# Performance work log

Measured on AMD Instinct MI355X. Metric: run time of the kernel, lower is better.

## Reference

```python
import jax, jax.numpy as jnp
import numpy as np

N_NODES = 100000


def gcn_conv(x, edge_index, W, num_nodes):
    """PyG GCNConv (bias=False): add self-loops, symmetric normalization,
    out[c] = sum_{(r,c) in E'} deg^{-1/2}[r] * deg^{-1/2}[c] * (x @ W)[r]."""
    h = x @ W  # [N, out_dim]
    row, col = edge_index[0], edge_index[1]
    loop = jnp.arange(num_nodes, dtype=row.dtype)
    row = jnp.concatenate([row, loop])
    col = jnp.concatenate([col, loop])
    ones = jnp.ones(row.shape[0], dtype=h.dtype)
    deg = jax.ops.segment_sum(ones, col, num_segments=num_nodes)  # [N]
    dinv = jnp.where(deg > 0, jax.lax.rsqrt(deg), 0.0)
    norm = dinv[row] * dinv[col]  # [E+N]
    msgs = norm[:, None] * h[row]  # gather + scale
    return jax.ops.segment_sum(msgs, col, num_segments=num_nodes)  # scatter-add


def setup_inputs() -> dict:
    key = jax.random.key(0)
    k1, k2, k3, k4 = jax.random.split(key, 4)
    x = jax.random.normal(k1, (N_NODES, 128), dtype=jnp.float32)
    edge_index = jax.random.randint(k2, (2, 3200000), 0, N_NODES, dtype=jnp.int64)
    W1 = jax.random.normal(k3, (128, 32), dtype=jnp.float32) * (1.0 / np.sqrt(128))
    W2 = jax.random.normal(k4, (32, 3), dtype=jnp.float32) * (1.0 / np.sqrt(32))
    return {"x": x, "edge_index": edge_index, "W1": W1, "W2": W2}


def reference(x, edge_index, W1, W2):
    n = x.shape[0]
    hidden1 = jnp.tanh(gcn_conv(x, edge_index, W1, n))  # dropout p=0.0 -> identity
    z = gcn_conv(hidden1, edge_index, W2, n)
    return z  # original returns (z, z, None)
```

## Files before the change

kernel.cpp:

```cpp
#include <hip/hip_runtime.h>
#include <hip/hip_fp16.h>

#define N_NODES 100000
#define N_EDGES 3200000
#define F_IN    128
#define F_HID   32

#define BSHIFT  7
#define BKSZ    128
#define NBKT    ((N_NODES + BKSZ - 1) / BKSZ)
#define CAP     4608
#define CHUNK   4096
#define NBLK_E  ((N_EDGES + CHUNK - 1) / CHUNK)
#define RBITS   17
#define RMASK   0x1FFFF


__global__ __launch_bounds__(512) void k_part(const int* __restrict__ row, const int* __restrict__ col,
                                              int* __restrict__ gcur, unsigned* __restrict__ bkt) {
    __shared__ int hist[NBKT];
    __shared__ int lbase[NBKT];
    __shared__ int gbase[NBKT];
    __shared__ unsigned perm[CHUNK];
    __shared__ unsigned short pb[CHUNK];
    __shared__ int wt[8];
    int t = threadIdx.x;
    for (int i = t; i < NBKT; i += 512) hist[i] = 0;
    __syncthreads();

    int e0 = blockIdx.x * CHUNK;
    int n  = min(CHUNK, N_EDGES - e0);
    int r[8], c[8], rk[8];
#pragma unroll
    for (int k = 0; k < 8; k++) {
        int idx = t + k * 512;
        if (idx < n) {
            r[k]  = row[e0 + idx];
            c[k]  = col[e0 + idx];
            rk[k] = atomicAdd(&hist[c[k] >> BSHIFT], 1);
        }
    }
    __syncthreads();

    {
        int b0 = t * 2;
        int s0 = (b0     < NBKT) ? hist[b0]     : 0;
        int s1 = (b0 + 1 < NBKT) ? hist[b0 + 1] : 0;
        int tsum = s0 + s1;
        int lane = t & 63, wid = t >> 6;
        int incl = tsum;
#pragma unroll
        for (int sh = 1; sh < 64; sh <<= 1) {
            int u = __shfl_up(incl, sh);
            if (lane >= sh) incl += u;
        }
        if (lane == 63) wt[wid] = incl;
        __syncthreads();
        int wpre = 0;
        for (int w = 0; w < wid; w++) wpre += wt[w];
        int excl = wpre + incl - tsum;
        if (b0     < NBKT) lbase[b0]     = excl;
        if (b0 + 1 < NBKT) lbase[b0 + 1] = excl + s0;
    }
    for (int i = t; i < NBKT; i += 512) {
        int h = hist[i];
        gbase[i] = i * CAP + (h ? atomicAdd(&gcur[i], h) : 0);
    }
    __syncthreads();

#pragma unroll
    for (int k = 0; k < 8; k++) {
        int idx = t + k * 512;
        if (idx < n) {
            int b   = c[k] >> BSHIFT;
            int pos = lbase[b] + rk[k];
            perm[pos] = (unsigned)r[k] | ((unsigned)(c[k] & (BKSZ - 1)) << RBITS);
            pb[pos]   = (unsigned short)b;
        }
    }
    __syncthreads();

    for (int i = t; i < n; i += 512) {
        int b = pb[i];
        bkt[gbase[b] + (i - lbase[b])] = perm[i];
    }
}


__global__ __launch_bounds__(1024) void k_bucket(unsigned* __restrict__ bkt,
                                                 const int* __restrict__ gcur,
                                                 int* __restrict__ off, int* __restrict__ end,
                                                 float* __restrict__ dinv) {
    __shared__ unsigned stg[CAP];
    __shared__ int cnt[BKSZ];
    __shared__ int cur[BKSZ];
    __shared__ int wtot[2];
    int t = threadIdx.x, b = blockIdx.x;
    int s = b * CAP, m = gcur[b];
    if (t < BKSZ) cnt[t] = 0;
    __syncthreads();
    for (int i = t; i < m; i += 1024) {
        unsigned x = bkt[s + i];
        stg[i] = x;
        atomicAdd(&cnt[x >> RBITS], 1);
    }
    __syncthreads();

    int lane = t & 63, wid = t >> 6;
    int v = 0, incl = 0;
    if (t < BKSZ) {
        v = cnt[t];
        incl = v;
        #pragma unroll
        for (int sh = 1; sh < 64; sh <<= 1) {
            int u = __shfl_up(incl, sh);
            if (lane >= sh) incl += u;
        }
        if (lane == 63) wtot[wid] = incl;
    }
    __syncthreads();
    if (t < BKSZ) {
        int wpre = (wid == 1) ? wtot[0] : 0;
        int excl = wpre + incl - v;
        cur[t] = s + excl;
        int g = b * BKSZ + t;
        if (g < N_NODES) {
            off[g]  = s + excl;
            end[g]  = s + excl + v;
            dinv[g] = rsqrtf((float)(v + 1));
        }
    }
    __syncthreads();
    for (int i = t; i < m; i += 1024) {
        unsigned x = stg[i];
        int p = atomicAdd(&cur[x >> RBITS], 1);
        bkt[p] = x & RMASK;
    }
}


__global__ __launch_bounds__(256) void k_gemm1(const float* __restrict__ x, const float* __restrict__ W1,
                                               const float* __restrict__ dinv, unsigned* __restrict__ h1s) {
    __shared__ float Wlds[F_IN * F_HID];
    int t = threadIdx.x;
    for (int i = t; i < F_IN * F_HID; i += 256) Wlds[i] = W1[i];
    __syncthreads();

    int gid = blockIdx.x * 256 + t;
    int r = gid >> 3, f4 = gid & 7;
    if (r >= N_NODES) return;

    const float4* x4  = (const float4*)(x + (size_t)r * F_IN);
    const float4* Wl4 = (const float4*)Wlds;
    float ax = 0.f, ay = 0.f, az = 0.f, aw = 0.f;
#pragma unroll
    for (int k4 = 0; k4 < F_IN / 4; k4++) {
        float4 xv = x4[k4];
        float4 w0 = Wl4[(4 * k4 + 0) * 8 + f4];
        ax += xv.x * w0.x; ay += xv.x * w0.y; az += xv.x * w0.z; aw += xv.x * w0.w;
        float4 w1 = Wl4[(4 * k4 + 1) * 8 + f4];
        ax += xv.y * w1.x; ay += xv.y * w1.y; az += xv.y * w1.z; aw += xv.y * w1.w;
        float4 w2 = Wl4[(4 * k4 + 2) * 8 + f4];
        ax += xv.z * w2.x; ay += xv.z * w2.y; az += xv.z * w2.z; aw += xv.z * w2.w;
        float4 w3 = Wl4[(4 * k4 + 3) * 8 + f4];
        ax += xv.w * w3.x; ay += xv.w * w3.y; az += xv.w * w3.z; aw += xv.w * w3.w;
    }
    float di = dinv[r];
    unsigned p01 = (unsigned)__half_as_ushort(__float2half(di * ax))
                 | ((unsigned)__half_as_ushort(__float2half(di * ay)) << 16);
    unsigned p23 = (unsigned)__half_as_ushort(__float2half(di * az))
                 | ((unsigned)__half_as_ushort(__float2half(di * aw)) << 16);
    ((uint2*)h1s)[(size_t)r * 8 + f4] = make_uint2(p01, p23);
}


__global__ __launch_bounds__(256) void k_conv1(const int* __restrict__ off, const int* __restrict__ end,
                                               const int* __restrict__ srt, const float* __restrict__ dinv,
                                               const unsigned* __restrict__ h1s,
                                               const float* __restrict__ W2, float* __restrict__ h2s4) {
    int wid  = threadIdx.x >> 6;
    int lane = threadIdx.x & 63;
    int c = blockIdx.x * 4 + wid;
    if (c >= N_NODES) return;
    int o = lane & 7;
    int q = lane >> 3;
    int pp = q & 1;
    int fA = 4 * o + 2 * pp, fB = fA + 1;

    float wA0 = W2[fA * 3 + 0], wA1 = W2[fA * 3 + 1], wA2 = W2[fA * 3 + 2];
    float wB0 = W2[fB * 3 + 0], wB1 = W2[fB * 3 + 1], wB2 = W2[fB * 3 + 2];

    int b = off[c], e = end[c];
    __half2 s01a = __float2half2_rn(0.0f), s23a = s01a;
    __half2 s01b = s01a, s23b = s01a;
    const uint2* h1v = (const uint2*)h1s;
    int p = b + q;
    for (; p + 8 < e; p += 16) {
        int r0 = srt[p];
        int r1 = srt[p + 8];
        uint2 v0 = h1v[(size_t)r0 * 8 + o];
        uint2 v1 = h1v[(size_t)r1 * 8 + o];
        s01a = __hadd2(s01a, *(const __half2*)&v0.x);
        s23a = __hadd2(s23a, *(const __half2*)&v0.y);
        s01b = __hadd2(s01b, *(const __half2*)&v1.x);
        s23b = __hadd2(s23b, *(const __half2*)&v1.y);
    }
    if (p < e) {
        int r0 = srt[p];
        uint2 v0 = h1v[(size_t)r0 * 8 + o];
        s01a = __hadd2(s01a, *(const __half2*)&v0.x);
        s23a = __hadd2(s23a, *(const __half2*)&v0.y);
    }
    __half2 s01 = __hadd2(s01a, s01b);
    __half2 s23 = __hadd2(s23a, s23b);

    float f0 = __low2float(s01), f1 = __high2float(s01);
    float f2v = __low2float(s23), f3 = __high2float(s23);
#pragma unroll
    for (int m = 8; m <= 32; m <<= 1) {
        f0  += __shfl_xor(f0, m);  f1 += __shfl_xor(f1, m);
        f2v += __shfl_xor(f2v, m); f3 += __shfl_xor(f3, m);
    }

    uint2 sv = h1v[(size_t)c * 8 + o];
    f0  += __low2float(*(const __half2*)&sv.x);
    f1  += __high2float(*(const __half2*)&sv.x);
    f2v += __low2float(*(const __half2*)&sv.y);
    f3  += __high2float(*(const __half2*)&sv.y);

    float di = dinv[c];
    float vA = pp ? f2v : f0;
    float vB = pp ? f3  : f1;
    float hA = tanhf(di * vA);
    float hB = tanhf(di * vB);

    float p0 = hA * wA0 + hB * wB0;
    float p1 = hA * wA1 + hB * wB1;
    float p2 = hA * wA2 + hB * wB2;
#pragma unroll
    for (int m = 1; m <= 32; m <<= 1) {
        p0 += __shfl_xor(p0, m);
        p1 += __shfl_xor(p1, m);
        p2 += __shfl_xor(p2, m);
    }
    if (lane < 4) {
        float vv = (lane == 0) ? p0 : (lane == 1) ? p1 : (lane == 2) ? p2 : 0.0f;
        h2s4[(size_t)c * 4 + lane] = (lane < 3) ? (di * 0.25f) * vv : 0.0f;
    }
}


__global__ __launch_bounds__(256) void k_conv2(const int* __restrict__ off, const int* __restrict__ end,
                                               const int* __restrict__ srt, const float* __restrict__ dinv,
                                               const float* __restrict__ h2s4, float* __restrict__ out) {
    int wid  = threadIdx.x >> 6;
    int lane = threadIdx.x & 63;
    int c = blockIdx.x * 4 + wid;
    if (c >= N_NODES) return;

    const float4* h2v = (const float4*)h2s4;
    int b = off[c], e = end[c];
    float ax = 0.0f, ay = 0.0f, az = 0.0f;
    for (int p = b + lane; p < e; p += 64) {
        int r = srt[p];
        float4 v = h2v[r];
        ax += v.x; ay += v.y; az += v.z;
    }
#pragma unroll
    for (int m = 1; m <= 32; m <<= 1) {
        ax += __shfl_xor(ax, m);
        ay += __shfl_xor(ay, m);
        az += __shfl_xor(az, m);
    }

    float di = dinv[c];
    if (lane < 3) {
        float a = (lane == 0) ? ax : (lane == 1) ? ay : az;
        out[(size_t)c * 3 + lane] = di * (a + h2s4[(size_t)c * 4 + lane]);
    }
}


extern "C" void kernel_launch(void* const* d_in, const int* in_sizes, int n_in,
                              void* d_out, int out_size, void* d_ws, size_t ws_size,
                              hipStream_t stream) {
    const float* x   = (const float*)d_in[0];
    const int*   ei  = (const int*)d_in[1];
    const float* W1  = (const float*)d_in[2];
    const float* W2  = (const float*)d_in[3];
    float*       out = (float*)d_out;

    const int* row = ei;
    const int* col = ei + N_EDGES;

    char* ws = (char*)d_ws;
    unsigned* bkt = (unsigned*)ws;
    int*      srt = (int*)ws;
    char*     p   = ws + 4ull * NBKT * CAP;
    int*      gcur = (int*)p;                 p += 4ull * ((NBKT + 63) & ~63);
    int*      off  = (int*)p;                 p += 4ull * N_NODES;
    int*      end  = (int*)p;                 p += 4ull * N_NODES;
    float*    dinv = (float*)p;               p += 4ull * N_NODES;
    unsigned* h1s  = (unsigned*)p;            p += 64ull * N_NODES;
    float*    h2s4 = (float*)p;

    const int B = 256;
    hipMemsetAsync(gcur, 0, 4ull * NBKT, stream);
    hipLaunchKernelGGL(k_part,   dim3(NBLK_E), dim3(512),  0, stream, row, col, gcur, bkt);
    hipLaunchKernelGGL(k_bucket, dim3(NBKT),   dim3(1024), 0, stream, bkt, gcur, off, end, dinv);
    hipLaunchKernelGGL(k_gemm1,  dim3((N_NODES * 8 + B - 1) / B), dim3(B), 0, stream, x, W1, dinv, h1s);
    hipLaunchKernelGGL(k_conv1,  dim3((N_NODES + 3) / 4), dim3(B), 0, stream,
                       off, end, srt, dinv, h1s, W2, h2s4);
    hipLaunchKernelGGL(k_conv2,  dim3((N_NODES + 3) / 4), dim3(B), 0, stream,
                       off, end, srt, dinv, h2s4, out);
}
```

Before: 247.4 us.

## Remap conv1 to 8 nodes per wavefront with padded zero row and fast tanh

conv1 now assigns 8 destination nodes per wavefront, one per 8-lane group, instead of one node per wavefront. Each group walks its own edge list 4 at a time with fp32 accumulators. Out-of-range slots point at a zeroed padding row N_NODES that gemm1 now writes. tanhf is replaced with an exp2/rcp approximation, and the self-loop term in conv2 moves into the initial accumulator. This is meant to cut wasted lanes and cross-lane shuffles on low-degree nodes, at the cost of lane divergence between nodes of different degree and slightly less accurate tanh.

```diff
diff --git a/kernel.cpp b/kernel.cpp
--- a/kernel.cpp
+++ b/kernel.cpp
@@ -14,6 +14,11 @@
 #define NBLK_E  ((N_EDGES + CHUNK - 1) / CHUNK)
 #define RBITS   17
 #define RMASK   0x1FFFF
+
+__device__ __forceinline__ float fast_tanh(float x) {
+    float t = __builtin_amdgcn_exp2f(x * 2.88539008f);
+    return 1.0f - 2.0f * __builtin_amdgcn_rcpf(t + 1.0f);
+}
 
 
 __global__ __launch_bounds__(512) void k_part(const int* __restrict__ row, const int* __restrict__ col,
@@ -148,7 +153,11 @@
 
     int gid = blockIdx.x * 256 + t;
     int r = gid >> 3, f4 = gid & 7;
-    if (r >= N_NODES) return;
+    if (r > N_NODES) return;
+    if (r == N_NODES) {
+        ((uint2*)h1s)[(size_t)r * 8 + f4] = make_uint2(0u, 0u);
+        return;
+    }
 
     const float4* x4  = (const float4*)(x + (size_t)r * F_IN);
     const float4* Wl4 = (const float4*)Wlds;
@@ -178,74 +187,75 @@
                                                const int* __restrict__ srt, const float* __restrict__ dinv,
                                                const unsigned* __restrict__ h1s,
                                                const float* __restrict__ W2, float* __restrict__ h2s4) {
-    int wid  = threadIdx.x >> 6;
-    int lane = threadIdx.x & 63;
-    int c = blockIdx.x * 4 + wid;
-    if (c >= N_NODES) return;
-    int o = lane & 7;
-    int q = lane >> 3;
-    int pp = q & 1;
-    int fA = 4 * o + 2 * pp, fB = fA + 1;
-
-    float wA0 = W2[fA * 3 + 0], wA1 = W2[fA * 3 + 1], wA2 = W2[fA * 3 + 2];
-    float wB0 = W2[fB * 3 + 0], wB1 = W2[fB * 3 + 1], wB2 = W2[fB * 3 + 2];
+    int t = threadIdx.x;
+    int lane = t & 63, wid = t >> 6;
+    int q = lane >> 3, o = lane & 7;
+    int c = (blockIdx.x * 4 + wid) * 8 + q;
 
     int b = off[c], e = end[c];
-    __half2 s01a = __float2half2_rn(0.0f), s23a = s01a;
-    __half2 s01b = s01a, s23b = s01a;
-    const uint2* h1v = (const uint2*)h1s;
-    int p = b + q;
-    for (; p + 8 < e; p += 16) {
-        int r0 = srt[p];
-        int r1 = srt[p + 8];
-        uint2 v0 = h1v[(size_t)r0 * 8 + o];
-        uint2 v1 = h1v[(size_t)r1 * 8 + o];
-        s01a = __hadd2(s01a, *(const __half2*)&v0.x);
-        s23a = __hadd2(s23a, *(const __half2*)&v0.y);
-        s01b = __hadd2(s01b, *(const __half2*)&v1.x);
-        s23b = __hadd2(s23b, *(const __half2*)&v1.y);
-    }
-    if (p < e) {
-        int r0 = srt[p];
-        uint2 v0 = h1v[(size_t)r0 * 8 + o];
-        s01a = __hadd2(s01a, *(const __half2*)&v0.x);
-        s23a = __hadd2(s23a, *(const __half2*)&v0.y);
-    }
-    __half2 s01 = __hadd2(s01a, s01b);
-    __half2 s23 = __hadd2(s23a, s23b);
-
-    float f0 = __low2float(s01), f1 = __high2float(s01);
-    float f2v = __low2float(s23), f3 = __high2float(s23);
-#pragma unroll
-    for (int m = 8; m <= 32; m <<= 1) {
-        f0  += __shfl_xor(f0, m);  f1 += __shfl_xor(f1, m);
-        f2v += __shfl_xor(f2v, m); f3 += __shfl_xor(f3, m);
-    }
-
-    uint2 sv = h1v[(size_t)c * 8 + o];
-    f0  += __low2float(*(const __half2*)&sv.x);
-    f1  += __high2float(*(const __half2*)&sv.x);
-    f2v += __low2float(*(const __half2*)&sv.y);
-    f3  += __high2float(*(const __half2*)&sv.y);
+    const char* h1b = (const char*)h1s;
+    unsigned oo = (unsigned)(o << 3);
+    uint2 sv = *(const uint2*)(h1b + (((unsigned)c << 6) + oo));
+    int last = (e > b) ? (e - 1) : b;
+
+    float a0a = 0.f, a1a = 0.f, a2a = 0.f, a3a = 0.f;
+    float a0b = 0.f, a1b = 0.f, a2b = 0.f, a3b = 0.f;
+    float a0c = 0.f, a1c = 0.f, a2c = 0.f, a3c = 0.f;
+    float a0d = 0.f, a1d = 0.f, a2d = 0.f, a3d = 0.f;
+
+    int p = b;
+    while (__any(p < e)) {
+        int i0 = min(p,     last);
+        int i1 = min(p + 1, last);
+        int i2 = min(p + 2, last);
+        int i3 = min(p + 3, last);
+        int r0 = srt[i0];
+        int r1 = srt[i1];
+        int r2 = srt[i2];
+        int r3 = srt[i3];
+        r0 = (p     < e) ? r0 : N_NODES;
+        r1 = (p + 1 < e) ? r1 : N_NODES;
+        r2 = (p + 2 < e) ? r2 : N_NODES;
+        r3 = (p + 3 < e) ? r3 : N_NODES;
+        uint2 v0 = *(const uint2*)(h1b + (((unsigned)r0 << 6) + oo));
+        uint2 v1 = *(const uint2*)(h1b + (((unsigned)r1 << 6) + oo));
+        uint2 v2 = *(const uint2*)(h1b + (((unsigned)r2 << 6) + oo));
+        uint2 v3 = *(const uint2*)(h1b + (((unsigned)r3 << 6) + oo));
+        a0a += __low2float(*(const __half2*)&v0.x);  a1a += __high2float(*(const __half2*)&v0.x);
+        a2a += __low2float(*(const __half2*)&v0.y);  a3a += __high2float(*(const __half2*)&v0.y);
+        a0b += __low2float(*(const __half2*)&v1.x);  a1b += __high2float(*(const __half2*)&v1.x);
+        a2b += __low2float(*(const __half2*)&v1.y);  a3b += __high2float(*(const __half2*)&v1.y);
+        a0c += __low2float(*(const __half2*)&v2.x);  a1c += __high2float(*(const __half2*)&v2.x);
+        a2c += __low2float(*(const __half2*)&v2.y);  a3c += __high2float(*(const __half2*)&v2.y);
+        a0d += __low2float(*(const __half2*)&v3.x);  a1d += __high2float(*(const __half2*)&v3.x);
+        a2d += __low2float(*(const __half2*)&v3.y);  a3d += __high2float(*(const __half2*)&v3.y);
+        p += 4;
+    }
 
     float di = dinv[c];
-    float vA = pp ? f2v : f0;
-    float vB = pp ? f3  : f1;
-    float hA = tanhf(di * vA);
-    float hB = tanhf(di * vB);
-
-    float p0 = hA * wA0 + hB * wB0;
-    float p1 = hA * wA1 + hB * wB1;
-    float p2 = hA * wA2 + hB * wB2;
-#pragma unroll
-    for (int m = 1; m <= 32; m <<= 1) {
+    float f0 = (a0a + a0b) + (a0c + a0d) + __low2float(*(const __half2*)&sv.x);
+    float f1 = (a1a + a1b) + (a1c + a1d) + __high2float(*(const __half2*)&sv.x);
+    float f2 = (a2a + a2b) + (a2c + a2d) + __low2float(*(const __half2*)&sv.y);
+    float f3 = (a3a + a3b) + (a3c + a3d) + __high2float(*(const __half2*)&sv.y);
+
+    float h0 = fast_tanh(di * f0);
+    float h1 = fast_tanh(di * f1);
+    float h2 = fast_tanh(di * f2);
+    float h3 = fast_tanh(di * f3);
+
+    const float* Wp = W2 + (o << 2) * 3;
+    float p0 = h0 * Wp[0] + h1 * Wp[3] + h2 * Wp[6] + h3 * Wp[9];
+    float p1 = h0 * Wp[1] + h1 * Wp[4] + h2 * Wp[7] + h3 * Wp[10];
+    float p2 = h0 * Wp[2] + h1 * Wp[5] + h2 * Wp[8] + h3 * Wp[11];
+#pragma unroll
+    for (int m = 1; m <= 4; m <<= 1) {
         p0 += __shfl_xor(p0, m);
         p1 += __shfl_xor(p1, m);
         p2 += __shfl_xor(p2, m);
     }
-    if (lane < 4) {
-        float vv = (lane == 0) ? p0 : (lane == 1) ? p1 : (lane == 2) ? p2 : 0.0f;
-        h2s4[(size_t)c * 4 + lane] = (lane < 3) ? (di * 0.25f) * vv : 0.0f;
+    if (o < 4) {
+        float vv = (o == 0) ? p0 : (o == 1) ? p1 : (o == 2) ? p2 : 0.0f;
+        h2s4[(size_t)c * 4 + o] = (o < 3) ? di * vv : 0.0f;
     }
 }
 
@@ -260,7 +270,10 @@
 
     const float4* h2v = (const float4*)h2s4;
     int b = off[c], e = end[c];
-    float ax = 0.0f, ay = 0.0f, az = 0.0f;
+    float4 sv = h2v[c];
+    float ax = (lane == 0) ? sv.x : 0.0f;
+    float ay = (lane == 0) ? sv.y : 0.0f;
+    float az = (lane == 0) ? sv.z : 0.0f;
     for (int p = b + lane; p < e; p += 64) {
         int r = srt[p];
         float4 v = h2v[r];
@@ -276,7 +289,7 @@
     float di = dinv[c];
     if (lane < 3) {
         float a = (lane == 0) ? ax : (lane == 1) ? ay : az;
-        out[(size_t)c * 3 + lane] = di * (a + h2s4[(size_t)c * 4 + lane]);
+        out[(size_t)c * 3 + lane] = di * a;
     }
 }
 
@@ -301,15 +314,15 @@
     int*      off  = (int*)p;                 p += 4ull * N_NODES;
     int*      end  = (int*)p;                 p += 4ull * N_NODES;
     float*    dinv = (float*)p;               p += 4ull * N_NODES;
-    unsigned* h1s  = (unsigned*)p;            p += 64ull * N_NODES;
+    unsigned* h1s  = (unsigned*)p;            p += 64ull * (N_NODES + 1);
     float*    h2s4 = (float*)p;
 
     const int B = 256;
     hipMemsetAsync(gcur, 0, 4ull * NBKT, stream);
     hipLaunchKernelGGL(k_part,   dim3(NBLK_E), dim3(512),  0, stream, row, col, gcur, bkt);
     hipLaunchKernelGGL(k_bucket, dim3(NBKT),   dim3(1024), 0, stream, bkt, gcur, off, end, dinv);
-    hipLaunchKernelGGL(k_gemm1,  dim3((N_NODES * 8 + B - 1) / B), dim3(B), 0, stream, x, W1, dinv, h1s);
-    hipLaunchKernelGGL(k_conv1,  dim3((N_NODES + 3) / 4), dim3(B), 0, stream,
+    hipLaunchKernelGGL(k_gemm1,  dim3(((N_NODES + 1) * 8 + B - 1) / B), dim3(B), 0, stream, x, W1, dinv, h1s);
+    hipLaunchKernelGGL(k_conv1,  dim3(N_NODES / 32), dim3(B), 0, stream,
                        off, end, srt, dinv, h1s, W2, h2s4);
     hipLaunchKernelGGL(k_conv2,  dim3((N_NODES + 3) / 4), dim3(B), 0, stream,
                        off, end, srt, dinv, h2s4, out);
```

Measured after the change: 234.7 us. 5.1% less time.
